# Kernel optimization log

Measured on AMD Instinct MI355X. Metric: run time of the kernel, lower is better.

Reference implementation:

```python
import jax, jax.numpy as jnp
import numpy as np

B, S, HID = 2, 2048, 2048
H, DN, DR, KVR, DV = 16, 128, 64, 512, 128
THETA = 10000.0
EPS = 1e-6
SCALE = (DN + DR) ** -0.5  # softmax_scale = q_head_dim ** -0.5 (rope_scaling is None)


def setup_inputs() -> dict:
    key = jax.random.key(0)
    ks = jax.random.split(key, 8)
    std = 0.02
    return {
        "hidden_states": jax.random.normal(ks[0], (B, S, HID), jnp.float32),
        "q_nope_weight": jax.random.normal(ks[1], (H * DN, HID), jnp.float32) * std,
        "q_pe_weight": jax.random.normal(ks[2], (H * DR, HID), jnp.float32) * std,
        "kv_a_weight": jax.random.normal(ks[3], (KVR + DR, HID), jnp.float32) * std,
        "kv_a_ln_weight": jnp.ones((KVR,), jnp.float32),
        "k_b_weight": jax.random.normal(ks[4], (H, DN, KVR), jnp.float32) * std,
        "v_b_weight": jax.random.normal(ks[5], (H, DV, KVR), jnp.float32) * std,
        "o_weight": jax.random.normal(ks[6], (HID, H * DV), jnp.float32) * std,
        "position_ids": jnp.arange(S, dtype=jnp.int32)[None, :],
    }


def _rotate_half(x):
    x1, x2 = jnp.split(x, 2, axis=-1)
    return jnp.concatenate((-x2, x1), axis=-1)


def _interleave(x):
    # torch: x.view(..., d//2, 2).transpose(-1, -2).reshape(..., d)
    *lead, d = x.shape
    x = x.reshape(*lead, d // 2, 2)
    x = jnp.swapaxes(x, -1, -2)
    return x.reshape(*lead, d)


def reference(hidden_states, q_nope_weight, q_pe_weight, kv_a_weight,
              kv_a_ln_weight, k_b_weight, v_b_weight, o_weight, position_ids):
    b, s, _ = hidden_states.shape
    # Q projections, split into no-rope and rope parts per head
    q_nope = jnp.einsum('bsh,ndh->bnsd', hidden_states, q_nope_weight.reshape(H, DN, HID))
    q_pe = jnp.einsum('bsh,ndh->bnsd', hidden_states, q_pe_weight.reshape(H, DR, HID))
    # Joint low-rank KV + shared rope-key projection (MQA-style)
    ckv_kpe = jnp.einsum('bsh,ch->bsc', hidden_states, kv_a_weight)  # [b,s,KVR+DR]
    ckv, k_pe = ckv_kpe[..., :KVR], ckv_kpe[..., KVR:]
    # RMSNorm over the compressed latent (kv_a_layernorm)
    var = jnp.mean(jnp.square(ckv), axis=-1, keepdims=True)
    ckv = ckv * jax.lax.rsqrt(var + EPS) * kv_a_ln_weight  # [b,s,KVR]
    # Rotary tables: cos/sin indexed by position_ids, broadcast over heads
    inv_freq = 1.0 / (THETA ** (jnp.arange(0, DR, 2, dtype=jnp.float32) / DR))
    t = position_ids.astype(jnp.float32)                 # [1,s]
    freqs = t[..., None] * inv_freq                      # [1,s,DR/2]
    emb = jnp.concatenate((freqs, freqs), axis=-1)       # [1,s,DR]
    cos = jnp.cos(emb)[:, None]                          # [1,1,s,DR]
    sin = jnp.sin(emb)[:, None]
    # Partial RoPE with the interleave permutation from apply_rotary_pos_emb
    q_pe = _interleave(q_pe)
    k_pe = _interleave(k_pe[:, None])                    # [b,1,s,DR]
    q_pe = q_pe * cos + _rotate_half(q_pe) * sin
    k_pe = (k_pe * cos + _rotate_half(k_pe) * sin)[:, 0] # [b,s,DR]
    # Weight absorption: fold k_b into q, attend directly in the latent space
    q_lat = jnp.einsum('bnsd,ndc->bnsc', q_nope, k_b_weight)  # [b,H,s,KVR]
    scores = (jnp.einsum('bnsc,btc->bnst', q_lat, ckv)
              + jnp.einsum('bnsd,btd->bnst', q_pe, k_pe)) * SCALE
    mask = jnp.tril(jnp.ones((s, s), dtype=bool))
    scores = jnp.where(mask, scores, jnp.finfo(scores.dtype).min)
    attn = jax.nn.softmax(scores, axis=-1)
    # Attention output in the latent space, then expand with v_b and o_proj
    out_lat = jnp.einsum('bnst,btc->bnsc', attn, ckv)         # [b,H,s,KVR]
    v_out = jnp.einsum('bnsc,ndc->bnsd', out_lat, v_b_weight) # [b,H,s,DV]
    v_out = v_out.transpose(0, 2, 1, 3).reshape(b, s, H * DV)
    return jnp.einsum('bsf,hf->bsh', v_out, o_weight)
```

## Files before the change

kernel.cpp:

```cpp
#include <hip/hip_runtime.h>
#include <hip/hip_bf16.h>


typedef __hip_bfloat16 bf16;
typedef __bf16 v8bf __attribute__((ext_vector_type(8)));
typedef float  v4f  __attribute__((ext_vector_type(4)));

#define S_    2048
#define SCALE_F 0.07216878364870322f

__device__ __forceinline__ void st1(float* p, float v){ *p = v; }
__device__ __forceinline__ void st1(bf16* p, float v){ *p = __float2bfloat16(v); }
__device__ __forceinline__ unsigned short bfb(float x){
  return __builtin_bit_cast(unsigned short, __float2bfloat16(x));
}
__device__ __forceinline__ unsigned pk2(float a, float b){
  return (unsigned)bfb(a) | ((unsigned)bfb(b) << 16);
}

typedef const void __attribute__((address_space(1)))* gas_t;
typedef void __attribute__((address_space(3)))* las_t;
__device__ __forceinline__ void g2l16(const void* g, void* l){
  __builtin_amdgcn_global_load_lds((gas_t)g, (las_t)l, 16, 0, 0);
}

__global__ void cossin_kernel(const int* __restrict__ pos, float* __restrict__ cosT,
                              float* __restrict__ sinT){
  int idx = blockIdx.x*256 + threadIdx.x;
  int i = idx & 31, s = idx >> 5;
  float t = (float)pos[s];
  float freq = t * powf(10000.0f, -(float)i/32.0f);
  cosT[idx] = cosf(freq);
  sinT[idx] = sinf(freq);
}

__global__ void castf2b_kernel(const float* __restrict__ src, bf16* __restrict__ dst, int n8){
  int i = blockIdx.x*256 + threadIdx.x;
  if (i >= n8) return;
  const float4* s = (const float4*)src;
  float4 a = s[2*i], b = s[2*i+1];
  uint4 o; o.x = pk2(a.x,a.y); o.y = pk2(a.z,a.w); o.z = pk2(b.x,b.y); o.w = pk2(b.z,b.w);
  ((uint4*)dst)[i] = o;
}

template<typename TC>
__global__ __launch_bounds__(256) void gemm2_kernel(
    const bf16* __restrict__ A, int lda, int aDiv, long aS1, long aS2,
    const bf16* __restrict__ W, int ldw, int wDiv, long wS1, long wS2,
    TC* __restrict__ C, int ldc, int cDiv, long cS1, long cS2,
    int N, int K, float alpha)
{
  int z = blockIdx.z;
  A += (long)(z/aDiv)*aS1 + (long)(z%aDiv)*aS2;
  W += (long)(z/wDiv)*wS1 + (long)(z%wDiv)*wS2;
  C += (long)(z/cDiv)*cS1 + (long)(z%cDiv)*cS2;
  __shared__ bf16 As[2][4096];
  __shared__ bf16 Ws[2][4096];
  const int tid = threadIdx.x;
  const int w = tid>>6, l = tid&63, g = l>>4, c16 = l&15;
  const int wr = (w>>1)*64, wc = (w&1)*64;
  const int row0 = blockIdx.y*128, col0 = blockIdx.x*128;

  const long aO1 = (long)(row0 + (tid>>2))*lda + (tid&3)*8;
  const long aO2 = (long)(row0 + 64 + (tid>>2))*lda + (tid&3)*8;
  int wr1 = col0 + (tid>>2);      if (wr1 > N-1) wr1 = N-1;
  int wr2 = col0 + 64 + (tid>>2); if (wr2 > N-1) wr2 = N-1;
  const long wO1 = (long)wr1*ldw + (tid&3)*8;
  const long wO2 = (long)wr2*ldw + (tid&3)*8;

  v4f acc[4][4];
  #pragma unroll
  for (int i=0;i<4;i++)
    #pragma unroll
    for (int j=0;j<4;j++) acc[i][j] = (v4f){0.f,0.f,0.f,0.f};

  auto STAGE = [&](int k0, int bsel){
    g2l16(A + aO1 + k0, &As[bsel][tid*8]);
    g2l16(A + aO2 + k0, &As[bsel][2048 + tid*8]);
    g2l16(W + wO1 + k0, &Ws[bsel][tid*8]);
    g2l16(W + wO2 + k0, &Ws[bsel][2048 + tid*8]);
  };
  STAGE(0, 0);
  __syncthreads();
  const int nk = K >> 5;
  for (int t=0; t<nk; ++t){
    const int cur = t & 1;
    if (t+1 < nk) STAGE((t+1)*32, cur^1);
    v8bf af[4], bw[4];
    #pragma unroll
    for (int mi=0;mi<4;mi++) af[mi] = *(const v8bf*)&As[cur][(wr+mi*16+c16)*32 + g*8];
    #pragma unroll
    for (int ni=0;ni<4;ni++) bw[ni] = *(const v8bf*)&Ws[cur][(wc+ni*16+c16)*32 + g*8];
    #pragma unroll
    for (int mi=0;mi<4;mi++)
      #pragma unroll
      for (int ni=0;ni<4;ni++)
        acc[mi][ni] = __builtin_amdgcn_mfma_f32_16x16x32_bf16(af[mi], bw[ni], acc[mi][ni], 0,0,0);
    __syncthreads();
  }
  #pragma unroll
  for (int mi=0;mi<4;mi++)
    #pragma unroll
    for (int ni=0;ni<4;ni++)
      #pragma unroll
      for (int r=0;r<4;r++){
        int row = row0 + wr + mi*16 + g*4 + r;
        int col = col0 + wc + ni*16 + c16;
        if (col < N) st1(C + (long)row*ldc + col, acc[mi][ni][r]*alpha);
      }
}

__global__ __launch_bounds__(256) void kbT_kernel(const float* __restrict__ kb,
                                                  bf16* __restrict__ kbT){
  __shared__ bf16 t[64][65];
  int h = blockIdx.z, c0 = blockIdx.x*64, d0 = blockIdx.y*64;
  const float* src = kb + ((long)h*128 + d0)*512 + c0;
  #pragma unroll
  for (int i=0;i<16;i++){
    int idx = i*256 + threadIdx.x;
    int dl = idx>>6, cl = idx&63;
    t[dl][cl] = __float2bfloat16(src[(long)dl*512 + cl]);
  }
  __syncthreads();
  bf16* dst = kbT + ((long)h*512 + c0)*128 + d0;
  #pragma unroll
  for (int i=0;i<16;i++){
    int idx = i*256 + threadIdx.x;
    int cl = idx>>6, dl = idx&63;
    dst[(long)cl*128 + dl] = t[dl][cl];
  }
}

__global__ __launch_bounds__(256) void tposeV_kernel(const bf16* __restrict__ Kb,
                                                     bf16* __restrict__ Kd){
  __shared__ bf16 t[64][65];
  int b = blockIdx.z, s0 = blockIdx.y*64, d0 = blockIdx.x*64;
  const bf16* src = Kb + ((long)(b*S_ + s0))*576 + d0;
  #pragma unroll
  for (int i=0;i<16;i++){
    int idx = i*256 + threadIdx.x;
    int sl = idx>>6, dl = idx&63;
    t[sl][dl] = src[(long)sl*576 + dl];
  }
  __syncthreads();
  bf16* dst = Kd + ((long)(b*512 + d0))*S_ + s0;
  #pragma unroll
  for (int i=0;i<16;i++){
    int idx = i*256 + threadIdx.x;
    int dl = idx>>6, sl = idx&63;
    dst[(long)dl*S_ + sl] = t[sl][dl];
  }
}

__global__ __launch_bounds__(256) void build_k_kernel(
    const bf16* __restrict__ ckv_kpe, const float* __restrict__ ln_w,
    const float* __restrict__ cosT, const float* __restrict__ sinT,
    bf16* __restrict__ Kb)
{
  int row = blockIdx.x;
  int s = row & (S_-1);
  int tid = threadIdx.x;
  const bf16* src = ckv_kpe + (long)row*576;
  float x0 = __bfloat162float(src[tid*2]), x1 = __bfloat162float(src[tid*2+1]);
  float ss = x0*x0 + x1*x1;
  #pragma unroll
  for (int o=32;o>=1;o>>=1) ss += __shfl_xor(ss, o, 64);
  __shared__ float wss[4];
  int wid = tid>>6, lane = tid&63;
  if (lane==0) wss[wid] = ss;
  __syncthreads();
  float tot = wss[0]+wss[1]+wss[2]+wss[3];
  float rs = rsqrtf(tot*(1.0f/512.0f) + 1e-6f);
  bf16* dst = Kb + (long)row*576;
  dst[tid*2]   = __float2bfloat16(x0*rs*ln_w[tid*2]);
  dst[tid*2+1] = __float2bfloat16(x1*rs*ln_w[tid*2+1]);
  if (tid < 32) {
    float p0 = __bfloat162float(src[512 + tid*2]);
    float p1 = __bfloat162float(src[512 + tid*2 + 1]);
    float c = cosT[s*32+tid], sn = sinT[s*32+tid];
    dst[512+tid] = __float2bfloat16(p0*c - p1*sn);
    dst[544+tid] = __float2bfloat16(p1*c + p0*sn);
  }
}

__global__ void rope_q_kernel(const bf16* __restrict__ qpe,
                              const float* __restrict__ cosT, const float* __restrict__ sinT,
                              bf16* __restrict__ Qb)
{
  int idx = blockIdx.x*256 + threadIdx.x;
  int i = idx & 31;
  int s = (idx >> 5) & (S_-1);
  int z = idx >> 16;
  int b = z >> 4, n = z & 15;
  long base = ((long)(b*S_+s))*1024 + n*64 + 2*i;
  float x0 = __bfloat162float(qpe[base]), x1 = __bfloat162float(qpe[base+1]);
  float c = cosT[s*32+i], sn = sinT[s*32+i];
  bf16* dst = Qb + ((long)z*S_ + s)*576;
  dst[512+i] = __float2bfloat16((x0*c - x1*sn)*SCALE_F);
  dst[544+i] = __float2bfloat16((x1*c + x0*sn)*SCALE_F);
}

#define K0_OFF 0
#define K1_OFF 36864
#define V0_OFF 73728
#define V1_OFF 106496
#define SX_OFF 139264
#define P_OFF  147456
#define SMEM_BYTES 152576

__global__ __launch_bounds__(512, 2) void attn_mfma_kernel(
    const bf16* __restrict__ Qg, const bf16* __restrict__ Kg,
    const bf16* __restrict__ Vdg, bf16* __restrict__ Og)
{
  extern __shared__ char smem[];
  const int tid = threadIdx.x;
  const int w   = tid >> 6;
  const int l   = tid & 63;
  const int g   = l >> 4;
  const int c16 = l & 15;
  const int rg  = w & 3;
  const int dh  = w >> 2;
  const int R   = rg * 16;
  const int Dh  = dh * 256;
  const int DQb = dh * 576;
  char* SX = smem + SX_OFF + rg*2048;
  char* Pp = smem + P_OFF  + rg*1280;

  const int lin = blockIdx.x;
  const int k8 = lin & 7;
  const int b  = k8 >> 2;
  const int u  = (lin >> 3)*4 + (k8 & 3);
  const int n  = u & 15;
  const int pr = u >> 4;
  const int z  = b*16 + n;

  const char* kb0 = (const char*)Kg  + (long)b*S_*1152;
  const char* vd0 = (const char*)Vdg + (long)b*512*S_*2;

  auto STAGE = [&](int tt, char* kd, char* vd){
    const char* ksrc = kb0 + (long)tt*32*1152;
    #pragma unroll
    for (int it=0; it<4; it++){
      int c = it*512 + tid;
      int kcol = c/72, j = c - kcol*72;
      g2l16(ksrc + kcol*1152 + ((j ^ (kcol&7))<<4), kd + c*16);
    }
    if (tid < 256){
      int c = 2048 + tid;
      int kcol = c/72, j = c - kcol*72;
      g2l16(ksrc + kcol*1152 + ((j ^ (kcol&7))<<4), kd + c*16);
    }
    const char* vsrc = vd0 + (long)tt*64;
    #pragma unroll
    for (int it=0; it<4; it++){
      int c = it*512 + tid;
      int s = c>>3, uu = (c&7) ^ (s&7);
      int d = 2*s + (uu>>2), j = uu&3;
      g2l16(vsrc + (long)d*(S_*2) + j*16, vd + c*16);
    }
  };

  for (int ph = 0; ph < 2; ++ph){
    const int qt = ph ? (31 - pr) : pr;
    const int q0 = qt * 64;

    v8bf qf[9];
    {
      const char* qgb = (const char*)Qg + ((long)z*S_ + q0 + R + c16)*1152 + DQb;
      #pragma unroll
      for (int kk=0;kk<9;kk++) qf[kk] = *(const v8bf*)(qgb + kk*64 + g*16);
    }
    v4f acc[16];
    #pragma unroll
    for (int i=0;i<16;i++) acc[i] = (v4f){0.f,0.f,0.f,0.f};
    float m2[2] = {-1e30f,-1e30f};
    float lsum[4] = {0.f,0.f,0.f,0.f};

    const int ntile = 2*qt + 2;
    __syncthreads();
    STAGE(0, smem + K0_OFF, smem + V0_OFF);

    for (int t = 0; t < ntile; ++t){
      asm volatile("s_waitcnt vmcnt(0)" ::: "memory");
      __syncthreads();
      char* kB = smem + ((t&1) ? K1_OFF : K0_OFF);
      char* vB = smem + ((t&1) ? V1_OFF : V0_OFF);
      if (t+1 < ntile)
        STAGE(t+1, smem + (((t+1)&1) ? K1_OFF : K0_OFF),
                    smem + (((t+1)&1) ? V1_OFF : V0_OFF));

      v4f s0 = (v4f){0.f,0.f,0.f,0.f}, s1 = (v4f){0.f,0.f,0.f,0.f};
      #pragma unroll
      for (int kk=0;kk<9;kk++){
        int j = dh*36 + kk*4 + g;
        v8bf kf0 = *(const v8bf*)(kB + c16*1152      + ((j ^ (c16&7))<<4));
        v8bf kf1 = *(const v8bf*)(kB + (16+c16)*1152 + ((j ^ (c16&7))<<4));
        s0 = __builtin_amdgcn_mfma_f32_16x16x32_bf16(qf[kk], kf0, s0, 0,0,0);
        s1 = __builtin_amdgcn_mfma_f32_16x16x32_bf16(qf[kk], kf1, s1, 0,0,0);
      }
      {
        const int pr0 = 2*(1-dh);
        #pragma unroll
        for (int rr=0; rr<2; rr++){
          int r = pr0 + rr;
          int row = g*4 + r;
          *(float*)(SX + row*128 + (((c16      + 4*row)&31)<<2)) = s0[r];
          *(float*)(SX + row*128 + (((16 + c16 + 4*row)&31)<<2)) = s1[r];
        }
      }
      asm volatile("s_waitcnt lgkmcnt(0)" ::: "memory");
      __builtin_amdgcn_s_barrier();
      __builtin_amdgcn_sched_barrier(0);
      {
        const int or0 = 2*dh;
        #pragma unroll
        for (int rr=0; rr<2; rr++){
          int r = or0 + rr;
          int row = g*4 + r;
          float v0 = s0[r] + *(const float*)(SX + row*128 + (((c16      + 4*row)&31)<<2));
          float v1 = s1[r] + *(const float*)(SX + row*128 + (((16 + c16 + 4*row)&31)<<2));
          if (t >= ntile-2){
            int kt0 = t*32;
            int qrow = q0 + R + row;
            if (kt0 + c16 > qrow)      v0 = -1e30f;
            if (kt0 + 16 + c16 > qrow) v1 = -1e30f;
          }
          float pm = fmaxf(v0, v1);
          pm = fmaxf(pm, __shfl_xor(pm, 1)); pm = fmaxf(pm, __shfl_xor(pm, 2));
          pm = fmaxf(pm, __shfl_xor(pm, 4)); pm = fmaxf(pm, __shfl_xor(pm, 8));
          float mn = fmaxf(m2[rr], pm);
          float alv = __expf(m2[rr] - mn);
          m2[rr] = mn;
          float p0 = __expf(v0 - mn);
          float p1 = __expf(v1 - mn);
          int bse = (row>>1)*128;
          int sw  = (row>>1)&7;
          *(unsigned short*)(Pp + bse + (((((row&1)<<2)|(c16>>3)) ^ sw)<<4) + (c16&7)*2) = bfb(p0);
          *(unsigned short*)(Pp + bse + (((((row&1)<<2)|(2+(c16>>3))) ^ sw)<<4) + (c16&7)*2) = bfb(p1);
          float sv = p0 + p1;
          sv += __shfl_xor(sv, 1); sv += __shfl_xor(sv, 2);
          sv += __shfl_xor(sv, 4); sv += __shfl_xor(sv, 8);
          if (c16 == 0) *(float2*)(Pp + 1024 + row*8) = make_float2(alv, sv);
        }
      }
      asm volatile("s_waitcnt lgkmcnt(0)" ::: "memory");
      __builtin_amdgcn_s_barrier();
      __builtin_amdgcn_sched_barrier(0);
      {
        float ax[4];
        #pragma unroll
        for (int r=0;r<4;r++){
          float2 ap = *(const float2*)(Pp + 1024 + (g*4+r)*8);
          lsum[r] = lsum[r]*ap.x + ap.y;
          ax[r] = ap.x;
        }
        if (ax[0]!=1.0f || ax[1]!=1.0f || ax[2]!=1.0f || ax[3]!=1.0f){
          #pragma unroll
          for (int cb=0;cb<16;cb++)
            #pragma unroll
            for (int r=0;r<4;r++) acc[cb][r] *= ax[r];
        }
        int prow = c16;
        int au = ((((prow&1)<<2)) | g) ^ ((prow>>1)&7);
        v8bf af = *(const v8bf*)(Pp + (prow>>1)*128 + (au<<4));
        #pragma unroll
        for (int cb=0;cb<16;cb++){
          int d = Dh + cb*16 + c16;
          int vu = ((((d&1)<<2)) | g) ^ ((d>>1)&7);
          v8bf vf = *(const v8bf*)(vB + (d>>1)*128 + (vu<<4));
          acc[cb] = __builtin_amdgcn_mfma_f32_16x16x32_bf16(af, vf, acc[cb], 0,0,0);
        }
      }
    }
    float inv[4];
    #pragma unroll
    for (int r=0;r<4;r++) inv[r] = 1.0f / lsum[r];
    #pragma unroll
    for (int cb=0;cb<16;cb++)
      #pragma unroll
      for (int r=0;r<4;r++){
        int qrow = q0 + R + g*4 + r;
        Og[((long)z*S_ + qrow)*512 + Dh + cb*16 + c16] = __float2bfloat16(acc[cb][r]*inv[r]);
      }
  }
}

extern "C" void kernel_launch(void* const* d_in, const int* in_sizes, int n_in,
                              void* d_out, int out_size, void* d_ws, size_t ws_size,
                              hipStream_t stream)
{
  const float* hidden = (const float*)d_in[0];
  const float* qn_w   = (const float*)d_in[1];
  const float* qpe_w  = (const float*)d_in[2];
  const float* kva_w  = (const float*)d_in[3];
  const float* ln_w   = (const float*)d_in[4];
  const float* kb_w   = (const float*)d_in[5];
  const float* vb_w   = (const float*)d_in[6];
  const float* o_w    = (const float*)d_in[7];
  const int*   pos    = (const int*)d_in[8];
  float* out = (float*)d_out;
  char* ws = (char*)d_ws;

  float* cosT  = (float*)(ws);
  float* sinT  = (float*)(ws + 262144);
  bf16*  ckvb  = (bf16*) (ws + 524288);
  bf16*  vbb   = (bf16*) (ws + 524288);
  bf16*  Qb    = (bf16*) (ws + 5242880);
  bf16*  ob    = (bf16*) (ws + 5242880);
  bf16*  Kb    = (bf16*) (ws + 80740352);
  bf16*  outl  = (bf16*) (ws + 85458944);
  bf16*  qnopeb= (bf16*) (ws + 85458944);
  bf16*  qpeb  = (bf16*) (ws + 102236160);
  bf16*  kbT   = (bf16*) (ws + 110624768);
  bf16*  hb    = (bf16*) (ws + 112721920);
  bf16*  qnb   = (bf16*) (ws + 129499136);
  bf16*  qpw   = (bf16*) (ws + 137887744);
  bf16*  kvab  = (bf16*) (ws + 142082048);
  bf16*  voutb = (bf16*) (ws + 152567808);
  bf16*  Kd    = (bf16*) (ws + 169345024);

  static_assert(sizeof(v8bf) == 16, "v8bf must be 16B");
  hipFuncSetAttribute((const void*)attn_mfma_kernel,
                      hipFuncAttributeMaxDynamicSharedMemorySize, SMEM_BYTES);

  cossin_kernel<<<256, 256, 0, stream>>>(pos, cosT, sinT);

  castf2b_kernel<<<4096, 256, 0, stream>>>(hidden, hb, 1048576);
  castf2b_kernel<<<2048, 256, 0, stream>>>(qn_w,  qnb, 524288);
  castf2b_kernel<<<1024, 256, 0, stream>>>(qpe_w, qpw, 262144);
  castf2b_kernel<<< 576, 256, 0, stream>>>(kva_w, kvab, 147456);

  gemm2_kernel<bf16><<<dim3(5,32,1),256,0,stream>>>(
      hb,2048, 1,0,0,  kvab,2048, 1,0,0,  ckvb,576, 1,0,0,  576,2048, 1.f);
  gemm2_kernel<bf16><<<dim3(16,32,1),256,0,stream>>>(
      hb,2048, 1,0,0,  qnb,2048, 1,0,0,  qnopeb,2048, 1,0,0,  2048,2048, 1.f);
  gemm2_kernel<bf16><<<dim3(8,32,1),256,0,stream>>>(
      hb,2048, 1,0,0,  qpw,2048, 1,0,0,  qpeb,1024, 1,0,0,  1024,2048, 1.f);

  kbT_kernel<<<dim3(8,2,16), 256, 0, stream>>>(kb_w, kbT);
  build_k_kernel<<<4096, 256, 0, stream>>>(ckvb, ln_w, cosT, sinT, Kb);
  castf2b_kernel<<<512, 256, 0, stream>>>(vb_w, vbb, 131072);
  tposeV_kernel<<<dim3(8,32,2), 256, 0, stream>>>(Kb, Kd);
  rope_q_kernel<<<8192, 256, 0, stream>>>(qpeb, cosT, sinT, Qb);

  gemm2_kernel<bf16><<<dim3(4,16,32),256,0,stream>>>(
      qnopeb,2048, 16,(long)S_*2048,128,  kbT,128, 16,0,65536,
      Qb,576, 1,(long)S_*576,0,  512,128, SCALE_F);

  attn_mfma_kernel<<<dim3(512), 512, SMEM_BYTES, stream>>>(Qb, Kb, Kd, outl);

  castf2b_kernel<<<2048, 256, 0, stream>>>(o_w, ob, 524288);

  gemm2_kernel<bf16><<<dim3(1,16,32),256,0,stream>>>(
      outl,512, 1,(long)S_*512,0,  vbb,512, 16,0,65536,
      voutb,2048, 16,(long)S_*2048,128,  128,512, 1.f);

  gemm2_kernel<float><<<dim3(16,32,1),256,0,stream>>>(
      voutb,2048, 1,0,0,  ob,2048, 1,0,0,  out,2048, 1,0,0,  2048,2048, 1.f);
}
```

Measured before the change: 636.5 us.

## Fuse three projection GEMMs, hoist attention staging offsets, lazily rescale softmax max

The three input projection GEMMs (q_nope, q_pe, kv_a) are merged into one proj3 kernel launch that picks its weight and output by block index, which removes two launches and fills the GPU with one larger grid. In the attention kernel, the K/V staging address offsets are computed once before the loop instead of on every tile. The online softmax now updates its running max only when the new max exceeds the old one by more than 8, skipping most rescale exponentials. That lazy rescale lets probabilities before normalisation reach up to e^8, which carries a small numeric risk in bf16 P and the fp32 accumulators.

```diff
diff --git a/kernel.cpp b/kernel.cpp
--- a/kernel.cpp
+++ b/kernel.cpp
@@ -110,6 +110,71 @@
       }
 }
 
+__global__ __launch_bounds__(256) void proj3_kernel(
+    const bf16* __restrict__ A,
+    const bf16* __restrict__ Wq, const bf16* __restrict__ Wp, const bf16* __restrict__ Wc,
+    bf16* __restrict__ Cq, bf16* __restrict__ Cp, bf16* __restrict__ Cc)
+{
+  const int bx = blockIdx.x;
+  const bf16* W; bf16* C; int ldc, N, col0;
+  if (bx < 16){ W = Wq; C = Cq; ldc = 2048; N = 2048; col0 = bx*128; }
+  else if (bx < 24){ W = Wp; C = Cp; ldc = 1024; N = 1024; col0 = (bx-16)*128; }
+  else { W = Wc; C = Cc; ldc = 576; N = 576; col0 = (bx-24)*128; }
+  __shared__ bf16 As[2][4096];
+  __shared__ bf16 Ws[2][4096];
+  const int tid = threadIdx.x;
+  const int w = tid>>6, l = tid&63, g = l>>4, c16 = l&15;
+  const int wr = (w>>1)*64, wc = (w&1)*64;
+  const int row0 = blockIdx.y*128;
+
+  const long aO1 = (long)(row0 + (tid>>2))*2048 + (tid&3)*8;
+  const long aO2 = (long)(row0 + 64 + (tid>>2))*2048 + (tid&3)*8;
+  int wr1 = col0 + (tid>>2);      if (wr1 > N-1) wr1 = N-1;
+  int wr2 = col0 + 64 + (tid>>2); if (wr2 > N-1) wr2 = N-1;
+  const long wO1 = (long)wr1*2048 + (tid&3)*8;
+  const long wO2 = (long)wr2*2048 + (tid&3)*8;
+
+  v4f acc[4][4];
+  #pragma unroll
+  for (int i=0;i<4;i++)
+    #pragma unroll
+    for (int j=0;j<4;j++) acc[i][j] = (v4f){0.f,0.f,0.f,0.f};
+
+  auto STAGE = [&](int k0, int bsel){
+    g2l16(A + aO1 + k0, &As[bsel][tid*8]);
+    g2l16(A + aO2 + k0, &As[bsel][2048 + tid*8]);
+    g2l16(W + wO1 + k0, &Ws[bsel][tid*8]);
+    g2l16(W + wO2 + k0, &Ws[bsel][2048 + tid*8]);
+  };
+  STAGE(0, 0);
+  __syncthreads();
+  for (int t=0; t<64; ++t){
+    const int cur = t & 1;
+    if (t+1 < 64) STAGE((t+1)*32, cur^1);
+    v8bf af[4], bw[4];
+    #pragma unroll
+    for (int mi=0;mi<4;mi++) af[mi] = *(const v8bf*)&As[cur][(wr+mi*16+c16)*32 + g*8];
+    #pragma unroll
+    for (int ni=0;ni<4;ni++) bw[ni] = *(const v8bf*)&Ws[cur][(wc+ni*16+c16)*32 + g*8];
+    #pragma unroll
+    for (int mi=0;mi<4;mi++)
+      #pragma unroll
+      for (int ni=0;ni<4;ni++)
+        acc[mi][ni] = __builtin_amdgcn_mfma_f32_16x16x32_bf16(af[mi], bw[ni], acc[mi][ni], 0,0,0);
+    __syncthreads();
+  }
+  #pragma unroll
+  for (int mi=0;mi<4;mi++)
+    #pragma unroll
+    for (int ni=0;ni<4;ni++)
+      #pragma unroll
+      for (int r=0;r<4;r++){
+        int row = row0 + wr + mi*16 + g*4 + r;
+        int col = col0 + wc + ni*16 + c16;
+        if (col < N) C[(long)row*ldc + col] = __float2bfloat16(acc[mi][ni][r]);
+      }
+}
+
 __global__ __launch_bounds__(256) void kbT_kernel(const float* __restrict__ kb,
                                                   bf16* __restrict__ kbT){
   __shared__ bf16 t[64][65];
@@ -237,27 +302,37 @@
   const char* kb0 = (const char*)Kg  + (long)b*S_*1152;
   const char* vd0 = (const char*)Vdg + (long)b*512*S_*2;
 
+  int kOffG[5], kOffL[5], vOffG[4], vOffL[4];
+  #pragma unroll
+  for (int it=0; it<4; it++){
+    int c = it*512 + tid;
+    int kcol = c/72, j = c - kcol*72;
+    kOffG[it] = kcol*1152 + ((j ^ (kcol&7))<<4);
+    kOffL[it] = c*16;
+  }
+  {
+    int c = 2048 + tid;
+    int kcol = c/72, j = c - kcol*72;
+    kOffG[4] = kcol*1152 + ((j ^ (kcol&7))<<4);
+    kOffL[4] = c*16;
+  }
+  #pragma unroll
+  for (int it=0; it<4; it++){
+    int c = it*512 + tid;
+    int s = c>>3, uu = (c&7) ^ (s&7);
+    int d = 2*s + (uu>>2), j = uu&3;
+    vOffG[it] = d*(S_*2) + j*16;
+    vOffL[it] = c*16;
+  }
+
   auto STAGE = [&](int tt, char* kd, char* vd){
-    const char* ksrc = kb0 + (long)tt*32*1152;
-    #pragma unroll
-    for (int it=0; it<4; it++){
-      int c = it*512 + tid;
-      int kcol = c/72, j = c - kcol*72;
-      g2l16(ksrc + kcol*1152 + ((j ^ (kcol&7))<<4), kd + c*16);
-    }
-    if (tid < 256){
-      int c = 2048 + tid;
-      int kcol = c/72, j = c - kcol*72;
-      g2l16(ksrc + kcol*1152 + ((j ^ (kcol&7))<<4), kd + c*16);
-    }
+    const char* ksrc = kb0 + (long)tt*36864;
+    #pragma unroll
+    for (int it=0; it<4; it++) g2l16(ksrc + kOffG[it], kd + kOffL[it]);
+    if (tid < 256) g2l16(ksrc + kOffG[4], kd + kOffL[4]);
     const char* vsrc = vd0 + (long)tt*64;
     #pragma unroll
-    for (int it=0; it<4; it++){
-      int c = it*512 + tid;
-      int s = c>>3, uu = (c&7) ^ (s&7);
-      int d = 2*s + (uu>>2), j = uu&3;
-      g2l16(vsrc + (long)d*(S_*2) + j*16, vd + c*16);
-    }
+    for (int it=0; it<4; it++) g2l16(vsrc + vOffG[it], vd + vOffL[it]);
   };
 
   for (int ph = 0; ph < 2; ++ph){
@@ -328,11 +403,13 @@
           float pm = fmaxf(v0, v1);
           pm = fmaxf(pm, __shfl_xor(pm, 1)); pm = fmaxf(pm, __shfl_xor(pm, 2));
           pm = fmaxf(pm, __shfl_xor(pm, 4)); pm = fmaxf(pm, __shfl_xor(pm, 8));
-          float mn = fmaxf(m2[rr], pm);
-          float alv = __expf(m2[rr] - mn);
-          m2[rr] = mn;
-          float p0 = __expf(v0 - mn);
-          float p1 = __expf(v1 - mn);
+          float alv = 1.0f;
+          if (pm > m2[rr] + 8.0f){
+            alv = __expf(m2[rr] - pm);
+            m2[rr] = pm;
+          }
+          float p0 = __expf(v0 - m2[rr]);
+          float p1 = __expf(v1 - m2[rr]);
           int bse = (row>>1)*128;
           int sw  = (row>>1)&7;
           *(unsigned short*)(Pp + bse + (((((row&1)<<2)|(c16>>3)) ^ sw)<<4) + (c16&7)*2) = bfb(p0);
@@ -430,12 +507,8 @@
   castf2b_kernel<<<1024, 256, 0, stream>>>(qpe_w, qpw, 262144);
   castf2b_kernel<<< 576, 256, 0, stream>>>(kva_w, kvab, 147456);
 
-  gemm2_kernel<bf16><<<dim3(5,32,1),256,0,stream>>>(
-      hb,2048, 1,0,0,  kvab,2048, 1,0,0,  ckvb,576, 1,0,0,  576,2048, 1.f);
-  gemm2_kernel<bf16><<<dim3(16,32,1),256,0,stream>>>(
-      hb,2048, 1,0,0,  qnb,2048, 1,0,0,  qnopeb,2048, 1,0,0,  2048,2048, 1.f);
-  gemm2_kernel<bf16><<<dim3(8,32,1),256,0,stream>>>(
-      hb,2048, 1,0,0,  qpw,2048, 1,0,0,  qpeb,1024, 1,0,0,  1024,2048, 1.f);
+  proj3_kernel<<<dim3(29,32,1),256,0,stream>>>(hb, qnb, qpw, kvab,
+                                               qnopeb, qpeb, ckvb);
 
   kbT_kernel<<<dim3(8,2,16), 256, 0, stream>>>(kb_w, kbT);
   build_k_kernel<<<4096, 256, 0, stream>>>(ckvb, ln_w, cosT, sinT, Kb);
```

Result: faster. 601.5 us (-5.5%).
